# Performance work log

Hardware: AMD Instinct MI355X
Metric: run time of the kernel (lower is better)

Reference implementation:

```python
import jax, jax.numpy as jnp
import numpy as np

H = 16            # num_attention_heads
LN_EPS = 1e-5


def setup_inputs() -> dict:
    key = jax.random.key(0)
    ks = jax.random.split(key, 12)
    B, S, D = 2, 2048, 1024
    w_scale = 1.0 / np.sqrt(D)
    inp = {
        "hidden_states": jax.random.normal(ks[0], (B, S, D), jnp.float32),
        "attention_mask": jnp.zeros((B, 1, S, S), jnp.float32),
        "extra_attn": jax.random.normal(ks[1], (B * H, S, S), jnp.float32) * 0.02,
        "Wq": jax.random.normal(ks[2], (D, D), jnp.float32) * w_scale,
        "bq": jnp.zeros((D,), jnp.float32),
        "Wk": jax.random.normal(ks[3], (D, D), jnp.float32) * w_scale,
        "bk": jnp.zeros((D,), jnp.float32),
        "Wv": jax.random.normal(ks[4], (D, D), jnp.float32) * w_scale,
        "bv": jnp.zeros((D,), jnp.float32),
        "Wo": jax.random.normal(ks[5], (D, D), jnp.float32) * w_scale,
        "bo": jnp.zeros((D,), jnp.float32),
        "ln_gamma": jnp.ones((D,), jnp.float32),
        "ln_beta": jnp.zeros((D,), jnp.float32),
    }
    return inp


def _split_heads(x, B, S):
    # [B,S,D] -> [B,H,S,head_dim]
    D = x.shape[-1]
    return x.reshape(B, S, H, D // H).transpose(0, 2, 1, 3)


def reference(hidden_states, attention_mask, extra_attn,
              Wq, bq, Wk, bk, Wv, bv, Wo, bo, ln_gamma, ln_beta):
    B, S, D = hidden_states.shape
    head_dim = D // H
    scaling = head_dim ** -0.5

    q = (hidden_states @ Wq.T + bq) * scaling
    k = hidden_states @ Wk.T + bk
    v = hidden_states @ Wv.T + bv
    q = _split_heads(q, B, S)
    k = _split_heads(k, B, S)
    v = _split_heads(v, B, S)

    # scores: [B,H,S,S]
    scores = jnp.einsum('bhqd,bhkd->bhqk', q, k)
    scores = scores + extra_attn.reshape(B, H, S, S)
    scores = scores + attention_mask  # broadcast over heads
    probs = jax.nn.softmax(scores, axis=-1)

    attn = jnp.einsum('bhqk,bhkd->bhqd', probs, v)  # [B,H,S,hd]
    attn = attn.transpose(0, 2, 1, 3).reshape(B, S, D)
    attn_out = attn @ Wo.T + bo

    # residual + LayerNorm
    x = hidden_states + attn_out
    mu = jnp.mean(x, axis=-1, keepdims=True)
    var = jnp.mean(jnp.square(x - mu), axis=-1, keepdims=True)
    out = (x - mu) * jax.lax.rsqrt(var + LN_EPS) * ln_gamma + ln_beta
    return out
```

## Files before the change

### kernel.cpp

```cpp
#include <hip/hip_runtime.h>
#include <hip/hip_bf16.h>
#include <math.h>

typedef __bf16 bf16;
typedef __bf16 bf16x4 __attribute__((ext_vector_type(4)));
typedef __bf16 bf16x8 __attribute__((ext_vector_type(8)));
typedef float floatx4 __attribute__((ext_vector_type(4)));

#define MFMA16(a, b, c) __builtin_amdgcn_mfma_f32_16x16x32_bf16(a, b, c, 0, 0, 0)

__global__ __launch_bounds__(256) void k_convert(
    const float* __restrict__ hid, const float* __restrict__ wq,
    const float* __restrict__ wk, const float* __restrict__ wv,
    const float* __restrict__ wo,
    bf16* __restrict__ hidb, bf16* __restrict__ wqkvb, bf16* __restrict__ wob) {
  int g = blockIdx.x * 256 + threadIdx.x;
  int idx = g * 4;
  const float* src;
  bf16* dst;
  if (idx < 4194304) {
    src = hid + idx; dst = hidb + idx;
  } else if (idx < 7340032) {
    const float* w = (idx < 5242880) ? wq : (idx < 6291456) ? wk : wv;
    src = w + ((idx - 4194304) & 1048575);
    dst = wqkvb + (idx - 4194304);
  } else {
    src = wo + (idx - 7340032); dst = wob + (idx - 7340032);
  }
  float4 v = *(const float4*)src;
  bf16x4 o;
  o[0] = (bf16)v.x; o[1] = (bf16)v.y; o[2] = (bf16)v.z; o[3] = (bf16)v.w;
  *(bf16x4*)dst = o;
}

__global__ __launch_bounds__(256) void k_qkv_gemm(
    const bf16* __restrict__ A, const bf16* __restrict__ Bt,
    const float* __restrict__ bq, const float* __restrict__ bk,
    const float* __restrict__ bv,
    bf16* __restrict__ Qb, bf16* __restrict__ Kb, bf16* __restrict__ Vb) {
  __shared__ __align__(16) bf16 Al[128 * 64];
  __shared__ __align__(16) bf16 Bl[128 * 64];
  int tid = threadIdx.x;
  int wave = tid >> 6, L = tid & 63, quad = L >> 4, ln = L & 15;
  int m0 = blockIdx.y * 128, n0 = blockIdx.x * 128;
  int wm = (wave >> 1) * 64, wn = (wave & 1) * 64;

  floatx4 zz = {0.f, 0.f, 0.f, 0.f};
  floatx4 acc[4][4];
#pragma unroll
  for (int i = 0; i < 4; i++)
#pragma unroll
    for (int j = 0; j < 4; j++) acc[i][j] = zz;

  for (int kk = 0; kk < 1024; kk += 64) {
    uint4 ar[4], br[4];
#pragma unroll
    for (int u = 0; u < 4; u++) {
      int ch = tid + u * 256;
      int r = ch >> 3, c8 = ch & 7;
      ar[u] = *(const uint4*)&A[(size_t)(m0 + r) * 1024 + kk + c8 * 8];
      br[u] = *(const uint4*)&Bt[(size_t)(n0 + r) * 1024 + kk + c8 * 8];
    }
    __syncthreads();
#pragma unroll
    for (int u = 0; u < 4; u++) {
      int ch = tid + u * 256;
      int r = ch >> 3, c8 = ch & 7;
      *(uint4*)&Al[r * 64 + c8 * 8] = ar[u];
      *(uint4*)&Bl[r * 64 + c8 * 8] = br[u];
    }
    __syncthreads();
#pragma unroll
    for (int t = 0; t < 64; t += 32) {
      bf16x8 af[4], bfr[4];
#pragma unroll
      for (int i = 0; i < 4; i++)
        af[i] = *(const bf16x8*)&Al[(wm + i * 16 + ln) * 64 + t + quad * 8];
#pragma unroll
      for (int j = 0; j < 4; j++)
        bfr[j] = *(const bf16x8*)&Bl[(wn + j * 16 + ln) * 64 + t + quad * 8];
#pragma unroll
      for (int i = 0; i < 4; i++)
#pragma unroll
        for (int j = 0; j < 4; j++) acc[i][j] = MFMA16(af[i], bfr[j], acc[i][j]);
    }
  }
#pragma unroll
  for (int i = 0; i < 4; i++) {
    int mbase = m0 + wm + i * 16 + quad * 4;
#pragma unroll
    for (int j = 0; j < 4; j++) {
      int n = n0 + wn + j * 16 + ln;
      int which = n >> 10, nn = n & 1023;
      float bias = (which == 0) ? bq[nn] : (which == 1) ? bk[nn] : bv[nn];
      int h = nn >> 6, d = nn & 63;
#pragma unroll
      for (int r = 0; r < 4; r++) {
        int mm = mbase + r;
        int b = mm >> 11, s = mm & 2047;
        int bh = b * 16 + h;
        float v = acc[i][j][r] + bias;
        if (which == 0)
          Qb[(size_t)bh * 131072 + s * 64 + d] = (bf16)(v * 0.125f);
        else if (which == 1)
          Kb[(size_t)bh * 131072 + s * 64 + d] = (bf16)v;
        else
          Vb[(size_t)bh * 131072 + (size_t)d * 2048 + s] = (bf16)v;
      }
    }
  }
}

__global__ __launch_bounds__(256) void k_attn(
    const bf16* __restrict__ Qb, const bf16* __restrict__ Kb,
    const bf16* __restrict__ Vb, const float* __restrict__ extra,
    const float* __restrict__ mask, bf16* __restrict__ ctx) {
  __shared__ __align__(16) bf16 Kl[64 * 64];
  __shared__ __align__(16) bf16 Vtl[64 * 64];
  __shared__ __align__(16) bf16 Pl[4][16 * 64];
  int tid = threadIdx.x;
  int wave = tid >> 6, L = tid & 63, quad = L >> 4, ln = L & 15;
  int bh = blockIdx.y, b = bh >> 4, h = bh & 15;
  int q0 = blockIdx.x * 64;
  int qrow = q0 + wave * 16;

  bf16x8 qf[2];
  qf[0] = *(const bf16x8*)&Qb[(size_t)bh * 131072 + (qrow + ln) * 64 + quad * 8];
  qf[1] = *(const bf16x8*)&Qb[(size_t)bh * 131072 + (qrow + ln) * 64 + 32 + quad * 8];

  float m_run[4], l_run[4];
  floatx4 zz = {0.f, 0.f, 0.f, 0.f};
  floatx4 Oacc[4];
#pragma unroll
  for (int r = 0; r < 4; r++) { m_run[r] = -INFINITY; l_run[r] = 0.f; }
#pragma unroll
  for (int dd = 0; dd < 4; dd++) Oacc[dd] = zz;

  const size_t ebase = (size_t)bh * 2048 * 2048;
  const size_t mbase = (size_t)b * 2048 * 2048;

  for (int k0 = 0; k0 < 2048; k0 += 64) {
    __syncthreads();
#pragma unroll
    for (int u = 0; u < 2; u++) {
      int ch = tid + u * 256;
      int row = ch >> 3, c8 = ch & 7;
      *(uint4*)&Kl[row * 64 + c8 * 8] =
          *(const uint4*)&Kb[(size_t)bh * 131072 + (k0 + row) * 64 + c8 * 8];
      *(uint4*)&Vtl[row * 64 + c8 * 8] =
          *(const uint4*)&Vb[(size_t)bh * 131072 + (size_t)row * 2048 + k0 + c8 * 8];
    }
    __syncthreads();

    floatx4 sc[4];
#pragma unroll
    for (int kb = 0; kb < 4; kb++) {
      bf16x8 kf0 = *(const bf16x8*)&Kl[(kb * 16 + ln) * 64 + quad * 8];
      bf16x8 kf1 = *(const bf16x8*)&Kl[(kb * 16 + ln) * 64 + 32 + quad * 8];
      floatx4 z = zz;
      z = MFMA16(qf[0], kf0, z);
      z = MFMA16(qf[1], kf1, z);
      sc[kb] = z;
    }
#pragma unroll
    for (int kb = 0; kb < 4; kb++) {
      int col = k0 + kb * 16 + ln;
#pragma unroll
      for (int r = 0; r < 4; r++) {
        int q = qrow + quad * 4 + r;
        sc[kb][r] += extra[ebase + (size_t)q * 2048 + col] +
                     mask[mbase + (size_t)q * 2048 + col];
      }
    }
#pragma unroll
    for (int r = 0; r < 4; r++) {
      float mloc = fmaxf(fmaxf(sc[0][r], sc[1][r]), fmaxf(sc[2][r], sc[3][r]));
      mloc = fmaxf(mloc, __shfl_xor(mloc, 1));
      mloc = fmaxf(mloc, __shfl_xor(mloc, 2));
      mloc = fmaxf(mloc, __shfl_xor(mloc, 4));
      mloc = fmaxf(mloc, __shfl_xor(mloc, 8));
      float m_new = fmaxf(m_run[r], mloc);
      float alpha = __expf(m_run[r] - m_new);
      m_run[r] = m_new;
      float rs = 0.f;
#pragma unroll
      for (int kb = 0; kb < 4; kb++) {
        float p = __expf(sc[kb][r] - m_new);
        sc[kb][r] = p;
        rs += p;
      }
      rs += __shfl_xor(rs, 1);
      rs += __shfl_xor(rs, 2);
      rs += __shfl_xor(rs, 4);
      rs += __shfl_xor(rs, 8);
      l_run[r] = l_run[r] * alpha + rs;
#pragma unroll
      for (int dd = 0; dd < 4; dd++) Oacc[dd][r] *= alpha;
#pragma unroll
      for (int kb = 0; kb < 4; kb++)
        Pl[wave][(quad * 4 + r) * 64 + kb * 16 + ln] = (bf16)sc[kb][r];
    }
    bf16x8 pf0 = *(const bf16x8*)&Pl[wave][ln * 64 + quad * 8];
    bf16x8 pf1 = *(const bf16x8*)&Pl[wave][ln * 64 + 32 + quad * 8];
#pragma unroll
    for (int dd = 0; dd < 4; dd++) {
      bf16x8 vf0 = *(const bf16x8*)&Vtl[(dd * 16 + ln) * 64 + quad * 8];
      bf16x8 vf1 = *(const bf16x8*)&Vtl[(dd * 16 + ln) * 64 + 32 + quad * 8];
      Oacc[dd] = MFMA16(pf0, vf0, Oacc[dd]);
      Oacc[dd] = MFMA16(pf1, vf1, Oacc[dd]);
    }
  }
#pragma unroll
  for (int dd = 0; dd < 4; dd++) {
#pragma unroll
    for (int r = 0; r < 4; r++) {
      int q = qrow + quad * 4 + r;
      float v = Oacc[dd][r] / l_run[r];
      ctx[((size_t)(b * 2048 + q)) * 1024 + h * 64 + dd * 16 + ln] = (bf16)v;
    }
  }
}

__global__ __launch_bounds__(256) void k_out_gemm(
    const bf16* __restrict__ A, const bf16* __restrict__ Bt,
    const float* __restrict__ bo, const float* __restrict__ hid,
    float* __restrict__ y) {
  __shared__ __align__(16) bf16 Al[128 * 64];
  __shared__ __align__(16) bf16 Bl[128 * 64];
  int tid = threadIdx.x;
  int wave = tid >> 6, L = tid & 63, quad = L >> 4, ln = L & 15;
  int m0 = blockIdx.y * 128, n0 = blockIdx.x * 128;
  int wm = (wave >> 1) * 64, wn = (wave & 1) * 64;

  floatx4 zz = {0.f, 0.f, 0.f, 0.f};
  floatx4 acc[4][4];
#pragma unroll
  for (int i = 0; i < 4; i++)
#pragma unroll
    for (int j = 0; j < 4; j++) acc[i][j] = zz;

  for (int kk = 0; kk < 1024; kk += 64) {
    uint4 ar[4], br[4];
#pragma unroll
    for (int u = 0; u < 4; u++) {
      int ch = tid + u * 256;
      int r = ch >> 3, c8 = ch & 7;
      ar[u] = *(const uint4*)&A[(size_t)(m0 + r) * 1024 + kk + c8 * 8];
      br[u] = *(const uint4*)&Bt[(size_t)(n0 + r) * 1024 + kk + c8 * 8];
    }
    __syncthreads();
#pragma unroll
    for (int u = 0; u < 4; u++) {
      int ch = tid + u * 256;
      int r = ch >> 3, c8 = ch & 7;
      *(uint4*)&Al[r * 64 + c8 * 8] = ar[u];
      *(uint4*)&Bl[r * 64 + c8 * 8] = br[u];
    }
    __syncthreads();
#pragma unroll
    for (int t = 0; t < 64; t += 32) {
      bf16x8 af[4], bfr[4];
#pragma unroll
      for (int i = 0; i < 4; i++)
        af[i] = *(const bf16x8*)&Al[(wm + i * 16 + ln) * 64 + t + quad * 8];
#pragma unroll
      for (int j = 0; j < 4; j++)
        bfr[j] = *(const bf16x8*)&Bl[(wn + j * 16 + ln) * 64 + t + quad * 8];
#pragma unroll
      for (int i = 0; i < 4; i++)
#pragma unroll
        for (int j = 0; j < 4; j++) acc[i][j] = MFMA16(af[i], bfr[j], acc[i][j]);
    }
  }
#pragma unroll
  for (int i = 0; i < 4; i++) {
    int mbase = m0 + wm + i * 16 + quad * 4;
#pragma unroll
    for (int j = 0; j < 4; j++) {
      int n = n0 + wn + j * 16 + ln;
      float bias = bo[n];
#pragma unroll
      for (int r = 0; r < 4; r++) {
        int mm = mbase + r;
        float v = acc[i][j][r] + bias + hid[(size_t)mm * 1024 + n];
        y[(size_t)mm * 1024 + n] = v;
      }
    }
  }
}

__global__ __launch_bounds__(256) void k_ln(float* __restrict__ y,
                                            const float* __restrict__ gamma,
                                            const float* __restrict__ beta) {
  int row = blockIdx.x, tid = threadIdx.x;
  float4 v = *(const float4*)&y[(size_t)row * 1024 + tid * 4];
  float s = v.x + v.y + v.z + v.w;
  float sq = v.x * v.x + v.y * v.y + v.z * v.z + v.w * v.w;
#pragma unroll
  for (int off = 32; off > 0; off >>= 1) {
    s += __shfl_xor(s, off);
    sq += __shfl_xor(sq, off);
  }
  __shared__ float red[8];
  int wave = tid >> 6, L = tid & 63;
  if (L == 0) { red[wave] = s; red[4 + wave] = sq; }
  __syncthreads();
  s = red[0] + red[1] + red[2] + red[3];
  sq = red[4] + red[5] + red[6] + red[7];
  float mu = s * (1.f / 1024.f);
  float var = sq * (1.f / 1024.f) - mu * mu;
  float rstd = rsqrtf(var + 1e-5f);
  float4 g = *(const float4*)&gamma[tid * 4];
  float4 be = *(const float4*)&beta[tid * 4];
  float4 o;
  o.x = (v.x - mu) * rstd * g.x + be.x;
  o.y = (v.y - mu) * rstd * g.y + be.y;
  o.z = (v.z - mu) * rstd * g.z + be.z;
  o.w = (v.w - mu) * rstd * g.w + be.w;
  *(float4*)&y[(size_t)row * 1024 + tid * 4] = o;
}

extern "C" void kernel_launch(void* const* d_in, const int* in_sizes, int n_in,
                              void* d_out, int out_size, void* d_ws,
                              size_t ws_size, hipStream_t stream) {
  const float* hid = (const float*)d_in[0];
  const float* mask = (const float*)d_in[1];
  const float* extra = (const float*)d_in[2];
  const float* Wq = (const float*)d_in[3];
  const float* bq = (const float*)d_in[4];
  const float* Wk = (const float*)d_in[5];
  const float* bk = (const float*)d_in[6];
  const float* Wv = (const float*)d_in[7];
  const float* bv = (const float*)d_in[8];
  const float* Wo = (const float*)d_in[9];
  const float* bo = (const float*)d_in[10];
  const float* gamma = (const float*)d_in[11];
  const float* beta = (const float*)d_in[12];
  float* out = (float*)d_out;

  char* ws = (char*)d_ws;
  bf16* hidb  = (bf16*)(ws);
  bf16* wqkvb = (bf16*)(ws + (8ull << 20));
  bf16* wob   = (bf16*)(ws + (14ull << 20));
  bf16* Qb    = (bf16*)(ws + (16ull << 20));
  bf16* Kb    = (bf16*)(ws + (24ull << 20));
  bf16* Vb    = (bf16*)(ws + (32ull << 20));
  bf16* ctx   = (bf16*)(ws + (40ull << 20));

  k_convert<<<8192, 256, 0, stream>>>(hid, Wq, Wk, Wv, Wo, hidb, wqkvb, wob);
  k_qkv_gemm<<<dim3(24, 32), 256, 0, stream>>>(hidb, wqkvb, bq, bk, bv, Qb, Kb, Vb);
  k_attn<<<dim3(32, 32), 256, 0, stream>>>(Qb, Kb, Vb, extra, mask, ctx);
  k_out_gemm<<<dim3(8, 32), 256, 0, stream>>>(ctx, wob, bo, hid, out);
  k_ln<<<4096, 256, 0, stream>>>(out, gamma, beta);
}
```

Measured before the change: 1.033 ms.

## Use direct global-to-LDS loads, double-buffer attention K/V, prefetch bias, retile out GEMM

The GEMMs and attention now load tiles with global_load_lds instead of staging through registers. Attention double-buffers the K/V tiles and prefetches the next extra_attn values one iteration ahead, so the loads overlap with compute. The output GEMM uses 64-row tiles to launch twice as many blocks, and the QKV epilogue writes V as 4-wide vectors. These changes target memory latency and occupancy, at the cost of more LDS use and more complex code.

```diff
diff --git a/kernel.cpp b/kernel.cpp
--- a/kernel.cpp
+++ b/kernel.cpp
@@ -8,6 +8,12 @@
 typedef float floatx4 __attribute__((ext_vector_type(4)));
 
 #define MFMA16(a, b, c) __builtin_amdgcn_mfma_f32_16x16x32_bf16(a, b, c, 0, 0, 0)
+
+__device__ __forceinline__ void gl_lds16(const bf16* g, bf16* l) {
+  __builtin_amdgcn_global_load_lds(
+      (const __attribute__((address_space(1))) void*)(g),
+      (__attribute__((address_space(3))) void*)(l), 16, 0, 0);
+}
 
 __global__ __launch_bounds__(256) void k_convert(
     const float* __restrict__ hid, const float* __restrict__ wq,
@@ -53,21 +59,14 @@
     for (int j = 0; j < 4; j++) acc[i][j] = zz;
 
   for (int kk = 0; kk < 1024; kk += 64) {
-    uint4 ar[4], br[4];
+    __syncthreads();
 #pragma unroll
     for (int u = 0; u < 4; u++) {
-      int ch = tid + u * 256;
+      int chw = u * 256 + wave * 64;
+      int ch = chw + L;
       int r = ch >> 3, c8 = ch & 7;
-      ar[u] = *(const uint4*)&A[(size_t)(m0 + r) * 1024 + kk + c8 * 8];
-      br[u] = *(const uint4*)&Bt[(size_t)(n0 + r) * 1024 + kk + c8 * 8];
-    }
-    __syncthreads();
-#pragma unroll
-    for (int u = 0; u < 4; u++) {
-      int ch = tid + u * 256;
-      int r = ch >> 3, c8 = ch & 7;
-      *(uint4*)&Al[r * 64 + c8 * 8] = ar[u];
-      *(uint4*)&Bl[r * 64 + c8 * 8] = br[u];
+      gl_lds16(&A[(size_t)(m0 + r) * 1024 + kk + c8 * 8], &Al[chw * 8]);
+      gl_lds16(&Bt[(size_t)(n0 + r) * 1024 + kk + c8 * 8], &Bl[chw * 8]);
     }
     __syncthreads();
 #pragma unroll
@@ -88,24 +87,28 @@
 #pragma unroll
   for (int i = 0; i < 4; i++) {
     int mbase = m0 + wm + i * 16 + quad * 4;
+    int b = mbase >> 11, s0 = mbase & 2047;
 #pragma unroll
     for (int j = 0; j < 4; j++) {
       int n = n0 + wn + j * 16 + ln;
       int which = n >> 10, nn = n & 1023;
       float bias = (which == 0) ? bq[nn] : (which == 1) ? bk[nn] : bv[nn];
       int h = nn >> 6, d = nn & 63;
-#pragma unroll
-      for (int r = 0; r < 4; r++) {
-        int mm = mbase + r;
-        int b = mm >> 11, s = mm & 2047;
-        int bh = b * 16 + h;
-        float v = acc[i][j][r] + bias;
-        if (which == 0)
-          Qb[(size_t)bh * 131072 + s * 64 + d] = (bf16)(v * 0.125f);
-        else if (which == 1)
-          Kb[(size_t)bh * 131072 + s * 64 + d] = (bf16)v;
-        else
-          Vb[(size_t)bh * 131072 + (size_t)d * 2048 + s] = (bf16)v;
+      int bh = b * 16 + h;
+      if (which == 2) {
+        bf16x4 v4;
+#pragma unroll
+        for (int r = 0; r < 4; r++) v4[r] = (bf16)(acc[i][j][r] + bias);
+        *(bf16x4*)&Vb[(size_t)bh * 131072 + (size_t)d * 2048 + s0] = v4;
+      } else {
+#pragma unroll
+        for (int r = 0; r < 4; r++) {
+          float v = acc[i][j][r] + bias;
+          if (which == 0)
+            Qb[(size_t)bh * 131072 + (s0 + r) * 64 + d] = (bf16)(v * 0.125f);
+          else
+            Kb[(size_t)bh * 131072 + (s0 + r) * 64 + d] = (bf16)v;
+        }
       }
     }
   }
@@ -115,14 +118,13 @@
     const bf16* __restrict__ Qb, const bf16* __restrict__ Kb,
     const bf16* __restrict__ Vb, const float* __restrict__ extra,
     const float* __restrict__ mask, bf16* __restrict__ ctx) {
-  __shared__ __align__(16) bf16 Kl[64 * 64];
-  __shared__ __align__(16) bf16 Vtl[64 * 64];
+  __shared__ __align__(16) bf16 Kl[2][64 * 64];
+  __shared__ __align__(16) bf16 Vtl[2][64 * 64];
   __shared__ __align__(16) bf16 Pl[4][16 * 64];
   int tid = threadIdx.x;
   int wave = tid >> 6, L = tid & 63, quad = L >> 4, ln = L & 15;
   int bh = blockIdx.y, b = bh >> 4, h = bh & 15;
-  int q0 = blockIdx.x * 64;
-  int qrow = q0 + wave * 16;
+  int qrow = blockIdx.x * 64 + wave * 16;
 
   bf16x8 qf[2];
   qf[0] = *(const bf16x8*)&Qb[(size_t)bh * 131072 + (qrow + ln) * 64 + quad * 8];
@@ -136,42 +138,70 @@
 #pragma unroll
   for (int dd = 0; dd < 4; dd++) Oacc[dd] = zz;
 
-  const size_t ebase = (size_t)bh * 2048 * 2048;
-  const size_t mbase = (size_t)b * 2048 * 2048;
-
-  for (int k0 = 0; k0 < 2048; k0 += 64) {
-    __syncthreads();
-#pragma unroll
-    for (int u = 0; u < 2; u++) {
-      int ch = tid + u * 256;
-      int row = ch >> 3, c8 = ch & 7;
-      *(uint4*)&Kl[row * 64 + c8 * 8] =
-          *(const uint4*)&Kb[(size_t)bh * 131072 + (k0 + row) * 64 + c8 * 8];
-      *(uint4*)&Vtl[row * 64 + c8 * 8] =
-          *(const uint4*)&Vb[(size_t)bh * 131072 + (size_t)row * 2048 + k0 + c8 * 8];
-    }
-    __syncthreads();
+  const float* eptr[4];
+  const float* mptr[4];
+#pragma unroll
+  for (int r = 0; r < 4; r++) {
+    int q = qrow + quad * 4 + r;
+    eptr[r] = extra + (size_t)bh * 4194304 + (size_t)q * 2048 + ln;
+    mptr[r] = mask + (size_t)b * 4194304 + (size_t)q * 2048 + ln;
+  }
+  float exc[4][4];
+#pragma unroll
+  for (int kb = 0; kb < 4; kb++)
+#pragma unroll
+    for (int r = 0; r < 4; r++) exc[kb][r] = eptr[r][kb * 16];
+
+#pragma unroll
+  for (int u = 0; u < 2; u++) {
+    int chw = u * 256 + wave * 64;
+    int ch = chw + L;
+    int row = ch >> 3, c8 = ch & 7;
+    gl_lds16(&Kb[(size_t)bh * 131072 + row * 64 + c8 * 8], &Kl[0][chw * 8]);
+    gl_lds16(&Vb[(size_t)bh * 131072 + (size_t)row * 2048 + c8 * 8], &Vtl[0][chw * 8]);
+  }
+
+  for (int t = 0; t < 32; t++) {
+    __syncthreads();
+    if (t < 31) {
+      int k0n = (t + 1) * 64;
+      bf16* Kn = Kl[(t + 1) & 1];
+      bf16* Vn = Vtl[(t + 1) & 1];
+#pragma unroll
+      for (int u = 0; u < 2; u++) {
+        int chw = u * 256 + wave * 64;
+        int ch = chw + L;
+        int row = ch >> 3, c8 = ch & 7;
+        gl_lds16(&Kb[(size_t)bh * 131072 + (k0n + row) * 64 + c8 * 8], &Kn[chw * 8]);
+        gl_lds16(&Vb[(size_t)bh * 131072 + (size_t)row * 2048 + k0n + c8 * 8], &Vn[chw * 8]);
+      }
+    }
+    const bf16* Kc = Kl[t & 1];
+    const bf16* Vc = Vtl[t & 1];
 
     floatx4 sc[4];
 #pragma unroll
     for (int kb = 0; kb < 4; kb++) {
-      bf16x8 kf0 = *(const bf16x8*)&Kl[(kb * 16 + ln) * 64 + quad * 8];
-      bf16x8 kf1 = *(const bf16x8*)&Kl[(kb * 16 + ln) * 64 + 32 + quad * 8];
+      bf16x8 kf0 = *(const bf16x8*)&Kc[(kb * 16 + ln) * 64 + quad * 8];
+      bf16x8 kf1 = *(const bf16x8*)&Kc[(kb * 16 + ln) * 64 + 32 + quad * 8];
       floatx4 z = zz;
       z = MFMA16(qf[0], kf0, z);
       z = MFMA16(qf[1], kf1, z);
       sc[kb] = z;
     }
-#pragma unroll
-    for (int kb = 0; kb < 4; kb++) {
-      int col = k0 + kb * 16 + ln;
-#pragma unroll
-      for (int r = 0; r < 4; r++) {
-        int q = qrow + quad * 4 + r;
-        sc[kb][r] += extra[ebase + (size_t)q * 2048 + col] +
-                     mask[mbase + (size_t)q * 2048 + col];
-      }
-    }
+    float en[4][4];
+    if (t < 31) {
+#pragma unroll
+      for (int kb = 0; kb < 4; kb++)
+#pragma unroll
+        for (int r = 0; r < 4; r++) en[kb][r] = eptr[r][64 + kb * 16];
+    }
+#pragma unroll
+    for (int kb = 0; kb < 4; kb++)
+#pragma unroll
+      for (int r = 0; r < 4; r++)
+        sc[kb][r] += exc[kb][r] + mptr[r][kb * 16];
+
 #pragma unroll
     for (int r = 0; r < 4; r++) {
       float mloc = fmaxf(fmaxf(sc[0][r], sc[1][r]), fmaxf(sc[2][r], sc[3][r]));
@@ -204,10 +234,18 @@
     bf16x8 pf1 = *(const bf16x8*)&Pl[wave][ln * 64 + 32 + quad * 8];
 #pragma unroll
     for (int dd = 0; dd < 4; dd++) {
-      bf16x8 vf0 = *(const bf16x8*)&Vtl[(dd * 16 + ln) * 64 + quad * 8];
-      bf16x8 vf1 = *(const bf16x8*)&Vtl[(dd * 16 + ln) * 64 + 32 + quad * 8];
+      bf16x8 vf0 = *(const bf16x8*)&Vc[(dd * 16 + ln) * 64 + quad * 8];
+      bf16x8 vf1 = *(const bf16x8*)&Vc[(dd * 16 + ln) * 64 + 32 + quad * 8];
       Oacc[dd] = MFMA16(pf0, vf0, Oacc[dd]);
       Oacc[dd] = MFMA16(pf1, vf1, Oacc[dd]);
+    }
+    if (t < 31) {
+#pragma unroll
+      for (int kb = 0; kb < 4; kb++)
+#pragma unroll
+        for (int r = 0; r < 4; r++) exc[kb][r] = en[kb][r];
+#pragma unroll
+      for (int r = 0; r < 4; r++) { eptr[r] += 64; mptr[r] += 64; }
     }
   }
 #pragma unroll
@@ -225,55 +263,54 @@
     const bf16* __restrict__ A, const bf16* __restrict__ Bt,
     const float* __restrict__ bo, const float* __restrict__ hid,
     float* __restrict__ y) {
-  __shared__ __align__(16) bf16 Al[128 * 64];
+  __shared__ __align__(16) bf16 Al[64 * 64];
   __shared__ __align__(16) bf16 Bl[128 * 64];
   int tid = threadIdx.x;
   int wave = tid >> 6, L = tid & 63, quad = L >> 4, ln = L & 15;
-  int m0 = blockIdx.y * 128, n0 = blockIdx.x * 128;
-  int wm = (wave >> 1) * 64, wn = (wave & 1) * 64;
+  int m0 = blockIdx.y * 64, n0 = blockIdx.x * 128;
+  int wm = (wave >> 1) * 32, wn = (wave & 1) * 64;
 
   floatx4 zz = {0.f, 0.f, 0.f, 0.f};
-  floatx4 acc[4][4];
-#pragma unroll
-  for (int i = 0; i < 4; i++)
+  floatx4 acc[2][4];
+#pragma unroll
+  for (int i = 0; i < 2; i++)
 #pragma unroll
     for (int j = 0; j < 4; j++) acc[i][j] = zz;
 
   for (int kk = 0; kk < 1024; kk += 64) {
-    uint4 ar[4], br[4];
+    __syncthreads();
+#pragma unroll
+    for (int u = 0; u < 2; u++) {
+      int chw = u * 256 + wave * 64;
+      int ch = chw + L;
+      int r = ch >> 3, c8 = ch & 7;
+      gl_lds16(&A[(size_t)(m0 + r) * 1024 + kk + c8 * 8], &Al[chw * 8]);
+    }
 #pragma unroll
     for (int u = 0; u < 4; u++) {
-      int ch = tid + u * 256;
+      int chw = u * 256 + wave * 64;
+      int ch = chw + L;
       int r = ch >> 3, c8 = ch & 7;
-      ar[u] = *(const uint4*)&A[(size_t)(m0 + r) * 1024 + kk + c8 * 8];
-      br[u] = *(const uint4*)&Bt[(size_t)(n0 + r) * 1024 + kk + c8 * 8];
-    }
-    __syncthreads();
-#pragma unroll
-    for (int u = 0; u < 4; u++) {
-      int ch = tid + u * 256;
-      int r = ch >> 3, c8 = ch & 7;
-      *(uint4*)&Al[r * 64 + c8 * 8] = ar[u];
-      *(uint4*)&Bl[r * 64 + c8 * 8] = br[u];
+      gl_lds16(&Bt[(size_t)(n0 + r) * 1024 + kk + c8 * 8], &Bl[chw * 8]);
     }
     __syncthreads();
 #pragma unroll
     for (int t = 0; t < 64; t += 32) {
-      bf16x8 af[4], bfr[4];
-#pragma unroll
-      for (int i = 0; i < 4; i++)
+      bf16x8 af[2], bfr[4];
+#pragma unroll
+      for (int i = 0; i < 2; i++)
         af[i] = *(const bf16x8*)&Al[(wm + i * 16 + ln) * 64 + t + quad * 8];
 #pragma unroll
       for (int j = 0; j < 4; j++)
         bfr[j] = *(const bf16x8*)&Bl[(wn + j * 16 + ln) * 64 + t + quad * 8];
 #pragma unroll
-      for (int i = 0; i < 4; i++)
+      for (int i = 0; i < 2; i++)
 #pragma unroll
         for (int j = 0; j < 4; j++) acc[i][j] = MFMA16(af[i], bfr[j], acc[i][j]);
     }
   }
 #pragma unroll
-  for (int i = 0; i < 4; i++) {
+  for (int i = 0; i < 2; i++) {
     int mbase = m0 + wm + i * 16 + quad * 4;
 #pragma unroll
     for (int j = 0; j < 4; j++) {
@@ -282,8 +319,7 @@
 #pragma unroll
       for (int r = 0; r < 4; r++) {
         int mm = mbase + r;
-        float v = acc[i][j][r] + bias + hid[(size_t)mm * 1024 + n];
-        y[(size_t)mm * 1024 + n] = v;
+        y[(size_t)mm * 1024 + n] = acc[i][j][r] + bias + hid[(size_t)mm * 1024 + n];
       }
     }
   }
@@ -350,6 +386,6 @@
   k_convert<<<8192, 256, 0, stream>>>(hid, Wq, Wk, Wv, Wo, hidb, wqkvb, wob);
   k_qkv_gemm<<<dim3(24, 32), 256, 0, stream>>>(hidb, wqkvb, bq, bk, bv, Qb, Kb, Vb);
   k_attn<<<dim3(32, 32), 256, 0, stream>>>(Qb, Kb, Vb, extra, mask, ctx);
-  k_out_gemm<<<dim3(8, 32), 256, 0, stream>>>(ctx, wob, bo, hid, out);
+  k_out_gemm<<<dim3(8, 64), 256, 0, stream>>>(ctx, wob, bo, hid, out);
   k_ln<<<4096, 256, 0, stream>>>(out, gamma, beta);
 }
```

Result: faster. 932.2 us (-9.8%).
